# Performance work log

Hardware: AMD Instinct MI355X
Metric: run time of the kernel (lower is better)

The kernel has to match this reference:

```python
import jax, jax.numpy as jnp
import numpy as np

S = 14
STEP = 1.0 / S
LAMBDA_COORD = 7.0
LAMBDA_NOOBJ = 0.2
LAMBDA_CLS = 1.5
EPS = 1e-06


def _abs_coords(boxes):
    # boxes: [N, S, S, 2, 5] -> [N, S, S, 2, 4] (x1,y1,x2,y2)
    ys, xs = jnp.meshgrid(jnp.arange(S, dtype=boxes.dtype), jnp.arange(S, dtype=boxes.dtype), indexing='ij')
    xg = xs[None, :, :, None]
    yg = ys[None, :, :, None]
    cx = (boxes[..., 0] + xg) * STEP
    cy = (boxes[..., 1] + yg) * STEP
    w = boxes[..., 2]
    h = boxes[..., 3]
    return jnp.stack([cx - w / 2, cy - h / 2, cx + w / 2, cy + h / 2], axis=-1)


def _iou(b1, b2):
    x1 = jnp.maximum(b1[..., 0], b2[..., 0])
    y1 = jnp.maximum(b1[..., 1], b2[..., 1])
    x2 = jnp.minimum(b1[..., 2], b2[..., 2])
    y2 = jnp.minimum(b1[..., 3], b2[..., 3])
    inter = jnp.clip(x2 - x1, 0) * jnp.clip(y2 - y1, 0)
    a1 = (b1[..., 2] - b1[..., 0]) * (b1[..., 3] - b1[..., 1])
    a2 = (b2[..., 2] - b2[..., 0]) * (b2[..., 3] - b2[..., 1])
    return inter / (a1 + a2 - inter + EPS)


def _ciou_loss(b1, b2):
    iou = _iou(b1, b2)
    cx1 = (b1[..., 0] + b1[..., 2]) / 2
    cy1 = (b1[..., 1] + b1[..., 3]) / 2
    cx2 = (b2[..., 0] + b2[..., 2]) / 2
    cy2 = (b2[..., 1] + b2[..., 3]) / 2
    center_dist = (cx1 - cx2) ** 2 + (cy1 - cy2) ** 2
    xc1 = jnp.minimum(b1[..., 0], b2[..., 0])
    yc1 = jnp.minimum(b1[..., 1], b2[..., 1])
    xc2 = jnp.maximum(b1[..., 2], b2[..., 2])
    yc2 = jnp.maximum(b1[..., 3], b2[..., 3])
    outer_diag = (xc2 - xc1) ** 2 + (yc2 - yc1) ** 2 + EPS
    w1 = jnp.clip(b1[..., 2] - b1[..., 0], EPS)
    h1 = jnp.clip(b1[..., 3] - b1[..., 1], EPS)
    w2 = jnp.clip(b2[..., 2] - b2[..., 0], EPS)
    h2 = jnp.clip(b2[..., 3] - b2[..., 1], EPS)
    v = (4.0 / jnp.pi ** 2) * (jnp.arctan(w2 / h2) - jnp.arctan(w1 / h1)) ** 2
    alpha = v / (1 - iou + v + EPS)
    ciou = iou - center_dist / outer_diag - alpha * v
    scale = jnp.clip(2 - w2 * h2, 1.0)
    return (1 - ciou) * scale


def setup_inputs() -> dict:
    key = jax.random.key(0)
    k1, k2 = jax.random.split(key)
    N = 4096
    pred = jax.random.uniform(k1, (N, S, S, 30), dtype=jnp.float32)
    target = jax.random.uniform(k2, (N, S, S, 30), dtype=jnp.float32)
    return {"pred": pred, "target": target}


def reference(pred, target):
    N = pred.shape[0]
    tb = target[..., :10].reshape(N, S, S, 2, 5)
    pb = pred[..., :10].reshape(N, S, S, 2, 5)
    tcls = target[..., 10:]
    pcls = pred[..., 10:]

    obj = tb[..., 4] > 0                      # [N,S,S,2]
    pabs = _abs_coords(pb)                    # [N,S,S,2,4]
    tabs = _abs_coords(tb)

    # responsible-box assignment: IoU of both pred boxes vs target box 0
    ious = _iou(pabs, tabs[..., 0:1, :])      # [N,S,S,2]
    max_i = jnp.argmax(ious, axis=-1)         # first-max tie-break, same as torch
    resp = max_i[..., None] == jnp.arange(2)  # [N,S,S,2] bool
    obj = obj & resp
    noobj = ~obj

    pconf = pb[..., 4]
    tconf = tb[..., 4]
    se = (pconf - tconf) ** 2
    noobj_loss = jnp.sum(se * noobj)
    obj_loss = jnp.sum(se * obj)

    bbox_loss = jnp.sum(_ciou_loss(pabs, tabs) * obj)

    sig = jnp.any(obj, axis=-1)               # [N,S,S]
    # torch F.binary_cross_entropy clamps log terms at -100
    logp = jnp.clip(jnp.log(pcls), -100.0)
    log1mp = jnp.clip(jnp.log1p(-pcls), -100.0)
    bce = -(tcls * logp + (1 - tcls) * log1mp)
    class_loss = jnp.sum(bce * sig[..., None]) * LAMBDA_CLS

    loss = obj_loss + LAMBDA_NOOBJ * noobj_loss + LAMBDA_COORD * bbox_loss + class_loss
    return loss / N
```

## Files before the change

### kernel.cpp

```cpp
#include <hip/hip_runtime.h>
#include <math.h>

namespace {
constexpr int SG = 14;
constexpr int NIMG = 4096;
constexpr int NCELLS = NIMG * SG * SG;
constexpr int CPB = 256;
constexpr int STRIDE = 11;
constexpr float STEPF = 1.0f / 14.0f;
constexpr float EPSF = 1e-6f;
constexpr float L_COORD = 7.0f;
constexpr float L_NOOBJ = 0.2f;
constexpr float L_CLS = 1.5f;
constexpr float INV_N = 1.0f / 4096.0f;
constexpr float FOUR_OVER_PI2 = 4.0f / (float)(M_PI * M_PI);
}

struct Box { float x1, y1, x2, y2; };

__device__ __forceinline__ float iou_fn(const Box& a, const Box& b) {
  float ix1 = fmaxf(a.x1, b.x1);
  float iy1 = fmaxf(a.y1, b.y1);
  float ix2 = fminf(a.x2, b.x2);
  float iy2 = fminf(a.y2, b.y2);
  float inter = fmaxf(ix2 - ix1, 0.0f) * fmaxf(iy2 - iy1, 0.0f);
  float a1 = (a.x2 - a.x1) * (a.y2 - a.y1);
  float a2 = (b.x2 - b.x1) * (b.y2 - b.y1);
  return __fdividef(inter, a1 + a2 - inter + EPSF);
}

__device__ __forceinline__ float bce_term(float pc, float tc) {
  const float lg   = fmaxf(__logf(pc), -100.0f);
  const float l1mp = fmaxf(__logf(1.0f - pc), -100.0f);
  return -(tc * lg + (1.0f - tc) * l1mp);
}

__global__ __launch_bounds__(256, 6) void yolo_loss_kernel(
    const float* __restrict__ pred, const float* __restrict__ tgt,
    float* __restrict__ out) {
  __shared__ float bp[CPB * STRIDE];
  __shared__ float bt[CPB * STRIDE];
  __shared__ float bce[CPB];
  __shared__ float sdata[4];

  const int tid = threadIdx.x;

  const float2* P2 = reinterpret_cast<const float2*>(pred) + (size_t)blockIdx.x * (CPB * 15);
  const float2* T2 = reinterpret_cast<const float2*>(tgt)  + (size_t)blockIdx.x * (CPB * 15);
  float2 pv[15], tv[15];
#pragma unroll
  for (int j = 0; j < 15; ++j) {
    pv[j] = P2[j * 256 + tid];
    tv[j] = T2[j * 256 + tid];
  }

  bce[tid] = 0.0f;
  __syncthreads();

#pragma unroll
  for (int j = 0; j < 15; ++j) {
    const int idx = j * 256 + tid;
    const int c = idx / 15;
    const int e = 2 * idx - 30 * c;
    const float2 v = pv[j];
    const float2 u = tv[j];
    if (e < 10) {
      bp[c * STRIDE + e] = v.x; bp[c * STRIDE + e + 1] = v.y;
      bt[c * STRIDE + e] = u.x; bt[c * STRIDE + e + 1] = u.y;
    } else {
      const float s = bce_term(v.x, u.x) + bce_term(v.y, u.y);
      atomicAdd(&bce[c], s);
    }
  }
  __syncthreads();

  float p[10], t[10];
#pragma unroll
  for (int k = 0; k < 10; ++k) {
    p[k] = bp[tid * STRIDE + k];
    t[k] = bt[tid * STRIDE + k];
  }

  const int cell = blockIdx.x * CPB + tid;
  const int rem = cell % (SG * SG);
  const float gx = (float)(rem % SG);
  const float gy = (float)(rem / SG);

  Box pa0, pa1, ta0, ta1;
  {
    float cx = (p[0] + gx) * STEPF, cy = (p[1] + gy) * STEPF, w = p[2], h = p[3];
    pa0 = {cx - 0.5f * w, cy - 0.5f * h, cx + 0.5f * w, cy + 0.5f * h};
    cx = (p[5] + gx) * STEPF; cy = (p[6] + gy) * STEPF; w = p[7]; h = p[8];
    pa1 = {cx - 0.5f * w, cy - 0.5f * h, cx + 0.5f * w, cy + 0.5f * h};
    cx = (t[0] + gx) * STEPF; cy = (t[1] + gy) * STEPF; w = t[2]; h = t[3];
    ta0 = {cx - 0.5f * w, cy - 0.5f * h, cx + 0.5f * w, cy + 0.5f * h};
    cx = (t[5] + gx) * STEPF; cy = (t[6] + gy) * STEPF; w = t[7]; h = t[8];
    ta1 = {cx - 0.5f * w, cy - 0.5f * h, cx + 0.5f * w, cy + 0.5f * h};
  }

  const float iou0 = iou_fn(pa0, ta0);
  const float iou1 = iou_fn(pa1, ta0);
  const bool m1 = iou1 > iou0;
  const bool obj0 = (t[4] > 0.0f) && !m1;
  const bool obj1 = (t[9] > 0.0f) && m1;
  const bool sig = obj0 || obj1;

  const float d0 = p[4] - t[4], d1 = p[9] - t[9];
  const float se0 = d0 * d0, se1 = d1 * d1;
  const float obj_loss   = (obj0 ? se0 : 0.0f) + (obj1 ? se1 : 0.0f);
  const float noobj_loss = (obj0 ? 0.0f : se0) + (obj1 ? 0.0f : se1);

  Box b1, b2;
  b1.x1 = m1 ? pa1.x1 : pa0.x1; b1.y1 = m1 ? pa1.y1 : pa0.y1;
  b1.x2 = m1 ? pa1.x2 : pa0.x2; b1.y2 = m1 ? pa1.y2 : pa0.y2;
  b2.x1 = m1 ? ta1.x1 : ta0.x1; b2.y1 = m1 ? ta1.y1 : ta0.y1;
  b2.x2 = m1 ? ta1.x2 : ta0.x2; b2.y2 = m1 ? ta1.y2 : ta0.y2;

  float bbox;
  {
    const float iou = iou_fn(b1, b2);
    const float cx1 = 0.5f * (b1.x1 + b1.x2), cy1 = 0.5f * (b1.y1 + b1.y2);
    const float cx2 = 0.5f * (b2.x1 + b2.x2), cy2 = 0.5f * (b2.y1 + b2.y2);
    const float cd = (cx1 - cx2) * (cx1 - cx2) + (cy1 - cy2) * (cy1 - cy2);
    const float ox1 = fminf(b1.x1, b2.x1), oy1 = fminf(b1.y1, b2.y1);
    const float ox2 = fmaxf(b1.x2, b2.x2), oy2 = fmaxf(b1.y2, b2.y2);
    const float od = (ox2 - ox1) * (ox2 - ox1) + (oy2 - oy1) * (oy2 - oy1) + EPSF;
    const float w1 = fmaxf(b1.x2 - b1.x1, EPSF), h1 = fmaxf(b1.y2 - b1.y1, EPSF);
    const float w2 = fmaxf(b2.x2 - b2.x1, EPSF), h2 = fmaxf(b2.y2 - b2.y1, EPSF);
    const float dat = atanf(__fdividef(w2, h2)) - atanf(__fdividef(w1, h1));
    const float v = FOUR_OVER_PI2 * dat * dat;
    const float alpha = __fdividef(v, 1.0f - iou + v + EPSF);
    const float ciou = iou - __fdividef(cd, od) - alpha * v;
    const float scale = fmaxf(2.0f - w2 * h2, 1.0f);
    bbox = sig ? (1.0f - ciou) * scale : 0.0f;
  }

  float acc = obj_loss + L_NOOBJ * noobj_loss + L_COORD * bbox
            + (sig ? L_CLS * bce[tid] : 0.0f);

#pragma unroll
  for (int off = 32; off > 0; off >>= 1) acc += __shfl_down(acc, off);

  const int lane = tid & 63;
  const int wid  = tid >> 6;
  if (lane == 0) sdata[wid] = acc;
  __syncthreads();
  if (tid == 0) {
    const float s = sdata[0] + sdata[1] + sdata[2] + sdata[3];
    atomicAdd(out, s * INV_N);
  }
}

extern "C" void kernel_launch(void* const* d_in, const int* in_sizes, int n_in,
                              void* d_out, int out_size, void* d_ws, size_t ws_size,
                              hipStream_t stream) {
  const float* pred = (const float*)d_in[0];
  const float* tgt  = (const float*)d_in[1];
  float* out = (float*)d_out;

  hipMemsetAsync(out, 0, (size_t)out_size * sizeof(float), stream);

  const int blocks = NCELLS / CPB;
  yolo_loss_kernel<<<blocks, CPB, 0, stream>>>(pred, tgt, out);
}
```

Measured before the change: 218.5 us.

## Stream inputs directly to LDS with global_load_lds and spread atomics over bins

Replaces the register-staged 256-thread tile load with 64-thread blocks that issue global_load_lds DMA straight into shared memory. Each lane then reads its full cell, including the class BCE terms, which removes the per-element shared atomics. The single contended output atomic becomes 1024 binned atomics in workspace, reduced by a second tiny kernel. This adds a kernel launch and yields smaller blocks with more of them; per-cell reads at a 30-float stride in LDS may cause bank conflicts.

```diff
diff --git a/kernel.cpp b/kernel.cpp
--- a/kernel.cpp
+++ b/kernel.cpp
@@ -3,10 +3,11 @@
 
 namespace {
 constexpr int SG = 14;
-constexpr int NIMG = 4096;
-constexpr int NCELLS = NIMG * SG * SG;
-constexpr int CPB = 256;
-constexpr int STRIDE = 11;
+constexpr int NCELLS = 4096 * SG * SG;
+constexpr int CPB = 64;
+constexpr int NBLK = NCELLS / CPB;
+constexpr int NBINS = 1024;
+constexpr int BYTES_PER_BLK = CPB * 30 * 4;
 constexpr float STEPF = 1.0f / 14.0f;
 constexpr float EPSF = 1e-6f;
 constexpr float L_COORD = 7.0f;
@@ -14,6 +15,16 @@
 constexpr float L_CLS = 1.5f;
 constexpr float INV_N = 1.0f / 4096.0f;
 constexpr float FOUR_OVER_PI2 = 4.0f / (float)(M_PI * M_PI);
+}
+
+#define AS1 __attribute__((address_space(1)))
+#define AS3 __attribute__((address_space(3)))
+
+__device__ __forceinline__ void gl_lds16(const void* g, void* l) {
+  __builtin_amdgcn_global_load_lds((const AS1 unsigned int*)g, (AS3 unsigned int*)l, 16, 0, 0);
+}
+__device__ __forceinline__ void gl_lds4(const void* g, void* l) {
+  __builtin_amdgcn_global_load_lds((const AS1 unsigned int*)g, (AS3 unsigned int*)l, 4, 0, 0);
 }
 
 struct Box { float x1, y1, x2, y2; };
@@ -35,53 +46,42 @@
   return -(tc * lg + (1.0f - tc) * l1mp);
 }
 
-__global__ __launch_bounds__(256, 6) void yolo_loss_kernel(
-    const float* __restrict__ pred, const float* __restrict__ tgt,
-    float* __restrict__ out) {
-  __shared__ float bp[CPB * STRIDE];
-  __shared__ float bt[CPB * STRIDE];
-  __shared__ float bce[CPB];
-  __shared__ float sdata[4];
+__global__ __launch_bounds__(64) void yolo_k1(const float* __restrict__ pred,
+                                              const float* __restrict__ tgt,
+                                              float* __restrict__ bins) {
+  __shared__ __align__(16) float pb[CPB * 30];
+  __shared__ __align__(16) float tb[CPB * 30];
 
-  const int tid = threadIdx.x;
-
-  const float2* P2 = reinterpret_cast<const float2*>(pred) + (size_t)blockIdx.x * (CPB * 15);
-  const float2* T2 = reinterpret_cast<const float2*>(tgt)  + (size_t)blockIdx.x * (CPB * 15);
-  float2 pv[15], tv[15];
-#pragma unroll
-  for (int j = 0; j < 15; ++j) {
-    pv[j] = P2[j * 256 + tid];
-    tv[j] = T2[j * 256 + tid];
-  }
-
-  bce[tid] = 0.0f;
-  __syncthreads();
+  const int lane = threadIdx.x;
+  const size_t base = (size_t)blockIdx.x * BYTES_PER_BLK;
+  const char* gp = (const char*)pred + base;
+  const char* gt = (const char*)tgt + base;
+  char* lp = (char*)pb;
+  char* lt = (char*)tb;
 
 #pragma unroll
-  for (int j = 0; j < 15; ++j) {
-    const int idx = j * 256 + tid;
-    const int c = idx / 15;
-    const int e = 2 * idx - 30 * c;
-    const float2 v = pv[j];
-    const float2 u = tv[j];
-    if (e < 10) {
-      bp[c * STRIDE + e] = v.x; bp[c * STRIDE + e + 1] = v.y;
-      bt[c * STRIDE + e] = u.x; bt[c * STRIDE + e + 1] = u.y;
-    } else {
-      const float s = bce_term(v.x, u.x) + bce_term(v.y, u.y);
-      atomicAdd(&bce[c], s);
-    }
+  for (int j = 0; j < 7; ++j) {
+    gl_lds16(gp + j * 1024 + lane * 16, lp + j * 1024);
+    gl_lds16(gt + j * 1024 + lane * 16, lt + j * 1024);
   }
-  __syncthreads();
+#pragma unroll
+  for (int j = 0; j < 2; ++j) {
+    gl_lds4(gp + 7168 + j * 256 + lane * 4, lp + 7168 + j * 256);
+    gl_lds4(gt + 7168 + j * 256 + lane * 4, lt + 7168 + j * 256);
+  }
+  asm volatile("s_waitcnt vmcnt(0)" ::: "memory");
+
+  const float2* pl = reinterpret_cast<const float2*>(pb + lane * 30);
+  const float2* tl = reinterpret_cast<const float2*>(tb + lane * 30);
 
   float p[10], t[10];
 #pragma unroll
-  for (int k = 0; k < 10; ++k) {
-    p[k] = bp[tid * STRIDE + k];
-    t[k] = bt[tid * STRIDE + k];
+  for (int k = 0; k < 5; ++k) {
+    const float2 v = pl[k]; p[2 * k] = v.x; p[2 * k + 1] = v.y;
+    const float2 u = tl[k]; t[2 * k] = u.x; t[2 * k + 1] = u.y;
   }
 
-  const int cell = blockIdx.x * CPB + tid;
+  const int cell = blockIdx.x * CPB + lane;
   const int rem = cell % (SG * SG);
   const float gx = (float)(rem % SG);
   const float gy = (float)(rem / SG);
@@ -135,20 +135,32 @@
     bbox = sig ? (1.0f - ciou) * scale : 0.0f;
   }
 
+  float cls = 0.0f;
+#pragma unroll
+  for (int k = 0; k < 10; ++k) {
+    const float2 v = pl[5 + k];
+    const float2 u = tl[5 + k];
+    cls += bce_term(v.x, u.x) + bce_term(v.y, u.y);
+  }
+
   float acc = obj_loss + L_NOOBJ * noobj_loss + L_COORD * bbox
-            + (sig ? L_CLS * bce[tid] : 0.0f);
+            + (sig ? L_CLS * cls : 0.0f);
 
 #pragma unroll
   for (int off = 32; off > 0; off >>= 1) acc += __shfl_down(acc, off);
+  if (lane == 0) atomicAdd(&bins[blockIdx.x & (NBINS - 1)], acc);
+}
 
-  const int lane = tid & 63;
-  const int wid  = tid >> 6;
-  if (lane == 0) sdata[wid] = acc;
+__global__ __launch_bounds__(256) void yolo_k2(const float* __restrict__ bins,
+                                               float* __restrict__ out) {
+  const int tid = threadIdx.x;
+  float s = bins[tid] + bins[tid + 256] + bins[tid + 512] + bins[tid + 768];
+#pragma unroll
+  for (int off = 32; off > 0; off >>= 1) s += __shfl_down(s, off);
+  __shared__ float sd[4];
+  if ((tid & 63) == 0) sd[tid >> 6] = s;
   __syncthreads();
-  if (tid == 0) {
-    const float s = sdata[0] + sdata[1] + sdata[2] + sdata[3];
-    atomicAdd(out, s * INV_N);
-  }
+  if (tid == 0) out[0] = (sd[0] + sd[1] + sd[2] + sd[3]) * INV_N;
 }
 
 extern "C" void kernel_launch(void* const* d_in, const int* in_sizes, int n_in,
@@ -156,10 +168,10 @@
                               hipStream_t stream) {
   const float* pred = (const float*)d_in[0];
   const float* tgt  = (const float*)d_in[1];
-  float* out = (float*)d_out;
+  float* out  = (float*)d_out;
+  float* bins = (float*)d_ws;
 
-  hipMemsetAsync(out, 0, (size_t)out_size * sizeof(float), stream);
-
-  const int blocks = NCELLS / CPB;
-  yolo_loss_kernel<<<blocks, CPB, 0, stream>>>(pred, tgt, out);
+  hipMemsetAsync(bins, 0, NBINS * sizeof(float), stream);
+  yolo_k1<<<NBLK, CPB, 0, stream>>>(pred, tgt, bins);
+  yolo_k2<<<1, 256, 0, stream>>>(bins, out);
 }
```

Result: faster. 207.2 us (-5.2%).
